# Kernel optimization log

Hardware: AMD Instinct MI355X
Metric: run time of the kernel (lower is better)

## Reference

```python
import jax, jax.numpy as jnp
import numpy as np

H = 512      # hidden_size
R = 47       # response_size
TR = 2       # treat_size
B = 128
T = 512


def _uniform(key, shape, k):
    return jax.random.uniform(key, shape, jnp.float32, -k, k)


def setup_inputs() -> dict:
    key = jax.random.key(0)
    ks = jax.random.split(key, 20)
    kinit = 1.0 / np.sqrt(H)
    inp = {
        "x_r": jax.random.normal(ks[0], (B, T, R), jnp.float32),
        "x_t": jax.random.normal(ks[1], (B, T, TR), jnp.float32),
        # r_rnn: 2-layer LSTM, input size R+TR=49 (torch gate order i,f,g,o)
        "r_Wih0": _uniform(ks[2], (4 * H, R + TR), kinit),
        "r_Whh0": _uniform(ks[3], (4 * H, H), kinit),
        "r_b0": _uniform(ks[4], (4 * H,), kinit),  # b_ih + b_hh fused
        "r_Wih1": _uniform(ks[5], (4 * H, H), kinit),
        "r_Whh1": _uniform(ks[6], (4 * H, H), kinit),
        "r_b1": _uniform(ks[7], (4 * H,), kinit),
        # t_rnn: 2-layer LSTM, input size 2*R+TR=96
        "t_Wih0": _uniform(ks[8], (4 * H, 2 * R + TR), kinit),
        "t_Whh0": _uniform(ks[9], (4 * H, H), kinit),
        "t_b0": _uniform(ks[10], (4 * H,), kinit),
        "t_Wih1": _uniform(ks[11], (4 * H, H), kinit),
        "t_Whh1": _uniform(ks[12], (4 * H, H), kinit),
        "t_b1": _uniform(ks[13], (4 * H,), kinit),
        # output linears
        "Wr": _uniform(ks[14], (R, H), kinit),
        "br": _uniform(ks[15], (R,), kinit),
        "Wt": _uniform(ks[16], (TR, H), kinit),
        "bt": _uniform(ks[17], (TR,), kinit),
    }
    return inp


def _lstm_cell(x, h, c, Wih, Whh, b):
    gates = x @ Wih.T + h @ Whh.T + b          # [B, 4H]
    i, f, g, o = jnp.split(gates, 4, axis=-1)
    c = jax.nn.sigmoid(f) * c + jax.nn.sigmoid(i) * jnp.tanh(g)
    h = jax.nn.sigmoid(o) * jnp.tanh(c)
    return h, c


def reference(x_r, x_t, r_Wih0, r_Whh0, r_b0, r_Wih1, r_Whh1, r_b1,
              t_Wih0, t_Whh0, t_b0, t_Wih1, t_Whh1, t_b1, Wr, br, Wt, bt):
    b = x_r.shape[0]
    z = jnp.zeros((b, H), x_r.dtype)
    carry0 = (z, z, z, z, z, z, z, z)  # (h,c) for 2 layers of r_rnn and t_rnn

    def step(carry, rt):
        hr0, cr0, hr1, cr1, ht0, ct0, ht1, ct1 = carry
        r, t = rt
        r_input = jnp.concatenate([r, t], axis=-1)          # [B, 49]
        hr0, cr0 = _lstm_cell(r_input, hr0, cr0, r_Wih0, r_Whh0, r_b0)
        hr1, cr1 = _lstm_cell(hr0, hr1, cr1, r_Wih1, r_Whh1, r_b1)
        r_out = hr1 @ Wr.T + br                             # [B, 47]
        t_input = jnp.concatenate([r_input, r_out], axis=-1)  # [B, 96]
        ht0, ct0 = _lstm_cell(t_input, ht0, ct0, t_Wih0, t_Whh0, t_b0)
        ht1, ct1 = _lstm_cell(ht0, ht1, ct1, t_Wih1, t_Whh1, t_b1)
        t_out = ht1 @ Wt.T + bt                             # [B, 2]
        return (hr0, cr0, hr1, cr1, ht0, ct0, ht1, ct1), (r_out, t_out)

    xs = (jnp.swapaxes(x_r, 0, 1), jnp.swapaxes(x_t, 0, 1))  # time-major [T,B,.]
    _, (r_seq, t_seq) = jax.lax.scan(step, carry0, xs)
    # back to batch-first, like the module's final permute(1,0,2)
    return jnp.swapaxes(r_seq, 0, 1), jnp.swapaxes(t_seq, 0, 1)
```

## Files before the change

kernel.cpp:

```cpp
#include <hip/hip_runtime.h>


typedef _Float16 half_t;
typedef _Float16 half8 __attribute__((ext_vector_type(8)));
typedef float floatx4 __attribute__((ext_vector_type(4)));
typedef unsigned long long ull_t;

#define OFF_W0 0
#define OFF_W1 131072
#define OFF_W2 1179648
#define OFF_W3 2228224
#define OFF_W4 3276800
#define OFF_W5 3407872
#define OFF_W6 3538944
#define OFF_W7 4587520
#define OFF_W8 5636096
#define OFF_W9 6684672
#define OFF_W10 6709248
#define W_TOTAL 6717440
#define H_BASE  6717440
#define RO_BASE 7241728
#define HALF_TOTAL 7258112
#define STATE_BYTE_OFF (H_BASE * 2)
#define C_BYTE_OFF (HALF_TOTAL * 2)
#define BAR_BYTE_OFF 15564800
#define X16_BYTE_OFF (BAR_BYTE_OFF + 4096)
#define WS_NEED_X16 ((unsigned long long)X16_BYTE_OFF + 8388608ull)
#define STATE_BYTES (X16_BYTE_OFF - STATE_BYTE_OFF)

#define NBLK 256
#define TOUT_BASE (128 * 512 * 47)

__device__ __forceinline__ floatx4 mfma16(half8 a, half8 b, floatx4 c) {
  return __builtin_amdgcn_mfma_f32_16x16x32_f16(a, b, c, 0, 0, 0);
}

__device__ __forceinline__ float fast_sig(float x) {
  x = fminf(fmaxf(x, -30.f), 30.f);
  float e = __expf(-x);
  return __builtin_amdgcn_rcpf(1.f + e);
}
__device__ __forceinline__ float fast_tanh(float x) {
  x = fminf(fmaxf(x, -15.f), 15.f);
  float e = __expf(-2.f * x);
  return (1.f - e) * __builtin_amdgcn_rcpf(1.f + e);
}

template <int N>
__device__ __forceinline__ void coh_stage(half8 (&bb)[N], const half_t* p) {
#pragma unroll
  for (int ks = 0; ks < N; ++ks)
    asm volatile("global_load_dwordx4 %0, %1, off sc0 sc1"
                 : "=v"(bb[ks])
                 : "v"(p + ks * 32));
}
__device__ __forceinline__ void drain_vm() {
  asm volatile("s_waitcnt vmcnt(0)" ::: "memory");
  __builtin_amdgcn_sched_barrier(0);
}

__device__ __forceinline__ void store_h4_coh(half_t* p, half_t h0, half_t h1,
                                             half_t h2, half_t h3) {
  union { ull_t u; _Float16 h[4]; } x;
  x.h[0] = h0; x.h[1] = h1; x.h[2] = h2; x.h[3] = h3;
  __hip_atomic_store((ull_t*)p, x.u, __ATOMIC_RELAXED,
                     __HIP_MEMORY_SCOPE_AGENT);
}

__device__ __forceinline__ void poll_llc(const unsigned* p, unsigned target,
                                         int pace) {
  for (;;) {
    unsigned v;
    asm volatile("global_load_dword %0, %1, off sc0 sc1\ns_waitcnt vmcnt(0)"
                 : "=v"(v) : "v"(p));
    if (v >= target) return;
    if (pace == 1) __builtin_amdgcn_s_sleep(1);
    else __builtin_amdgcn_s_sleep(3);
  }
}

template <int NT, int NSEG, int LDW>
__device__ __forceinline__ void gemm_staged(const half_t* __restrict__ W,
                                            const int* wrow,
                                            const half8 (&bb)[NSEG], int lk,
                                            int l15, floatx4 (&acc)[NT]) {
#pragma unroll
  for (int ks = 0; ks < NSEG; ++ks) {
    const int kb = ks * 32 + lk;
#pragma unroll
    for (int n = 0; n < NT; ++n) {
      half8 a = *(const half8*)(W + (long)(wrow[n] + l15) * LDW + kb);
      acc[n] = mfma16(a, bb[ks], acc[n]);
    }
  }
}

__device__ __forceinline__ void gemm_plain2(const half_t* __restrict__ W,
                                            const int* wrow,
                                            const half_t* __restrict__ xb,
                                            int lk, int l15, floatx4 (&acc)[4]) {
#pragma unroll
  for (int ks = 0; ks < 2; ++ks) {
    const int kb = ks * 32 + lk;
    half8 b = *(const half8*)(xb + kb);
#pragma unroll
    for (int n = 0; n < 4; ++n) {
      half8 a = *(const half8*)(W + (long)(wrow[n] + l15) * 64 + kb);
      acc[n] = mfma16(a, b, acc[n]);
    }
  }
}

__device__ __forceinline__ void gemm_xf(const float* __restrict__ xr,
                                        const float* __restrict__ xt, int t,
                                        int batch, const half_t* __restrict__ W,
                                        const int* wrow, int lk, int l15,
                                        floatx4 (&acc)[4]) {
#pragma unroll
  for (int ks = 0; ks < 2; ++ks) {
    const int kb = ks * 32 + lk;
    half8 b;
    const long base = (long)batch * 512 + t;
#pragma unroll
    for (int j = 0; j < 8; ++j) {
      const int kk = kb + j;
      float f = 0.f;
      if (kk < 47) f = xr[base * 47 + kk];
      else if (kk < 49) f = xt[base * 2 + (kk - 47)];
      b[j] = (half_t)f;
    }
#pragma unroll
    for (int n = 0; n < 4; ++n) {
      half8 a = *(const half8*)(W + (long)(wrow[n] + l15) * 64 + kb);
      acc[n] = mfma16(a, b, acc[n]);
    }
  }
}

__device__ __forceinline__ void lstm_epi_sw(floatx4 (&acc)[4],
                                            const float* __restrict__ bias,
                                            float* __restrict__ cst,
                                            half_t* __restrict__ hdst,
                                            int batch, int hcol0) {
  const floatx4 bI = *(const floatx4*)(bias + hcol0);
  const floatx4 bF = *(const floatx4*)(bias + 512 + hcol0);
  const floatx4 bG = *(const floatx4*)(bias + 1024 + hcol0);
  const floatx4 bO = *(const floatx4*)(bias + 1536 + hcol0);
  const int off = batch * 512 + hcol0;
  floatx4 cold = *(floatx4*)(cst + off);
  floatx4 cn;
  half_t hn[4];
#pragma unroll
  for (int r = 0; r < 4; ++r) {
    const float gi = acc[0][r] + bI[r];
    const float gf = acc[1][r] + bF[r];
    const float gg = acc[2][r] + bG[r];
    const float go = acc[3][r] + bO[r];
    cn[r] = fast_sig(gf) * cold[r] + fast_sig(gi) * fast_tanh(gg);
    hn[r] = (half_t)(fast_sig(go) * fast_tanh(cn[r]));
  }
  *(floatx4*)(cst + off) = cn;
  store_h4_coh(hdst + off, hn[0], hn[1], hn[2], hn[3]);
}

__global__ __launch_bounds__(256, 1) void adrnn_persist(
    const float* __restrict__ xr, const float* __restrict__ xt,
    const float* __restrict__ b_r0, const float* __restrict__ b_r1,
    const float* __restrict__ b_t0, const float* __restrict__ b_t1,
    const float* __restrict__ brv, const float* __restrict__ btv,
    half_t* __restrict__ w16, float* __restrict__ cbase,
    float* __restrict__ out, unsigned* bar, const half_t* __restrict__ x16,
    int use_x16) {
  const int bid = blockIdx.x;
  const int tid = threadIdx.x;
  const int lane = tid & 63;
  const int w = tid >> 6;
  const int l15 = lane & 15;
  const int q = lane >> 4;
  const int lk = q * 8;
  half_t* H = w16 + H_BASE;
  half_t* RO = w16 + RO_BASE;
#define HB(cell, p) (H + (((cell)*2 + (p)) << 16))

  const int stage = (bid & 7) >> 1;
  const int csHi = bid & 1;
  const int bh = (bid >> 3) & 1;
  const int csLo = bid >> 4;
  const int cs = csHi * 16 + csLo;
  const int sub = cs * 2 + bh;
  const int c0 = cs * 16;
  const int batch = bh * 64 + w * 16 + l15;
  const int hboff = batch * 512;
  const int hcol0 = c0 + q * 4;
  const int sd = (stage == 0) ? 0 : (stage == 1) ? 1 : (stage == 2) ? 3 : 4;
  int wrow[4] = {c0, 512 + c0, 1024 + c0, 1536 + c0};
  const int flat = sub * 4 + w;

  unsigned* larr = bar + (bid & 7) * 32;
  unsigned* garr = bar + 256;
  unsigned* lgen = bar + 288 + (bid & 7) * 32;

  for (int k = 0; k < 517; ++k) {
    const int par = k & 1, pq = par ^ 1;
    const int t = k - sd;
    if (t >= 0 && t < 512) {
      floatx4 acc[4] = {};
      if (stage == 0) {
        half8 b0[16];
        coh_stage<16>(b0, HB(0, pq) + hboff + lk);
        drain_vm();
        if (use_x16)
          gemm_plain2(w16 + OFF_W0, wrow, x16 + t * 8192 + batch * 64, lk, l15, acc);
        else
          gemm_xf(xr, xt, t, batch, w16 + OFF_W0, wrow, lk, l15, acc);
        gemm_staged<4, 16, 512>(w16 + OFF_W1, wrow, b0, lk, l15, acc);
        lstm_epi_sw(acc, b_r0, cbase + 0 * 65536, HB(0, par), batch, hcol0);
      } else if (stage == 1) {
        half8 b0[16], b1[16];
        coh_stage<16>(b0, HB(0, pq) + hboff + lk);
        coh_stage<16>(b1, HB(1, pq) + hboff + lk);
        drain_vm();
        gemm_staged<4, 16, 512>(w16 + OFF_W2, wrow, b0, lk, l15, acc);
        gemm_staged<4, 16, 512>(w16 + OFF_W3, wrow, b1, lk, l15, acc);
        lstm_epi_sw(acc, b_r1, cbase + 1 * 65536, HB(1, par), batch, hcol0);
      } else if (stage == 2) {
        half8 bro[2], b2[16];
        coh_stage<2>(bro, RO + pq * 8192 + batch * 64 + lk);
        coh_stage<16>(b2, HB(2, pq) + hboff + lk);
        drain_vm();
        if (use_x16)
          gemm_plain2(w16 + OFF_W4, wrow, x16 + t * 8192 + batch * 64, lk, l15, acc);
        else
          gemm_xf(xr, xt, t, batch, w16 + OFF_W4, wrow, lk, l15, acc);
        gemm_staged<4, 2, 64>(w16 + OFF_W5, wrow, bro, lk, l15, acc);
        gemm_staged<4, 16, 512>(w16 + OFF_W6, wrow, b2, lk, l15, acc);
        lstm_epi_sw(acc, b_t0, cbase + 2 * 65536, HB(2, par), batch, hcol0);
      } else {
        half8 b0[16], b1[16];
        coh_stage<16>(b0, HB(2, pq) + hboff + lk);
        coh_stage<16>(b1, HB(3, pq) + hboff + lk);
        drain_vm();
        gemm_staged<4, 16, 512>(w16 + OFF_W7, wrow, b0, lk, l15, acc);
        gemm_staged<4, 16, 512>(w16 + OFF_W8, wrow, b1, lk, l15, acc);
        lstm_epi_sw(acc, b_t1, cbase + 3 * 65536, HB(3, par), batch, hcol0);
      }
    }
    if (stage == 0 && flat < 32) {
      if (flat < 24) {
        const int tr = k - 2;
        if (tr >= 0 && tr < 512) {
          const int n = flat >> 3, btl = flat & 7;
          const int rb = btl * 16 + l15;
          half8 bs[16];
          coh_stage<16>(bs, HB(1, pq) + rb * 512 + lk);
          drain_vm();
          int wr1[1] = {n * 16};
          floatx4 accr[1] = {};
          gemm_staged<1, 16, 512>(w16 + OFF_W9, wr1, bs, lk, l15, accr);
          const int wc0 = n * 16 + q * 4;
          half_t ro4[4];
#pragma unroll
          for (int r = 0; r < 4; ++r) {
            const int wc = wc0 + r;
            float v = 0.f;
            if (wc < 47) {
              v = accr[0][r] + brv[wc];
              out[((long)rb * 512 + tr) * 47 + wc] = v;
            }
            ro4[r] = (half_t)v;
          }
          store_h4_coh(RO + par * 8192 + rb * 64 + wc0, ro4[0], ro4[1], ro4[2], ro4[3]);
        }
      } else {
        const int tt = k - 5;
        if (tt >= 0 && tt < 512) {
          const int btl = flat - 24;
          const int rb = btl * 16 + l15;
          half8 bs[16];
          coh_stage<16>(bs, HB(3, pq) + rb * 512 + lk);
          drain_vm();
          int wt1[1] = {0};
          floatx4 accw[1] = {};
          gemm_staged<1, 16, 512>(w16 + OFF_W10, wt1, bs, lk, l15, accw);
          if (q == 0) {
#pragma unroll
            for (int r = 0; r < 2; ++r)
              out[TOUT_BASE + ((long)rb * 512 + tt) * 2 + r] = accw[0][r] + btv[r];
          }
        }
      }
    }
    asm volatile("s_waitcnt vmcnt(0)" ::: "memory");
    __syncthreads();
    if (tid == 0) {
      const unsigned ku = (unsigned)k + 1u;
      (void)__hip_atomic_fetch_add(larr, 1u, __ATOMIC_RELAXED,
                                   __HIP_MEMORY_SCOPE_AGENT);
      if (bid < 8) {
        poll_llc(larr, 32u * ku, 1);
        (void)__hip_atomic_fetch_add(garr, 1u, __ATOMIC_RELAXED,
                                     __HIP_MEMORY_SCOPE_AGENT);
        poll_llc(garr, 8u * ku, 1);
        (void)__hip_atomic_fetch_add(lgen, 1u, __ATOMIC_RELAXED,
                                     __HIP_MEMORY_SCOPE_AGENT);
      } else {
        poll_llc(lgen, ku, 3);
      }
    }
    __syncthreads();
    asm volatile("" ::: "memory");
  }
#undef HB
}

__global__ __launch_bounds__(256) void conv_w(
    const float* __restrict__ rWih0, const float* __restrict__ rWhh0,
    const float* __restrict__ rWih1, const float* __restrict__ rWhh1,
    const float* __restrict__ tWih0, const float* __restrict__ tWhh0,
    const float* __restrict__ tWih1, const float* __restrict__ tWhh1,
    const float* __restrict__ Wr, const float* __restrict__ Wt,
    half_t* __restrict__ w16) {
  const int idx = blockIdx.x * 256 + threadIdx.x;
  if (idx >= W_TOTAL) return;
  float v = 0.f;
  if (idx < OFF_W1) {
    int n = idx >> 6, kk = idx & 63;
    if (kk < 49) v = rWih0[n * 49 + kk];
  } else if (idx < OFF_W2) {
    int r = idx - OFF_W1; v = rWhh0[r];
  } else if (idx < OFF_W3) {
    int r = idx - OFF_W2; v = rWih1[r];
  } else if (idx < OFF_W4) {
    int r = idx - OFF_W3; v = rWhh1[r];
  } else if (idx < OFF_W5) {
    int r = idx - OFF_W4; int n = r >> 6, kk = r & 63;
    if (kk < 49) v = tWih0[n * 96 + kk];
  } else if (idx < OFF_W6) {
    int r = idx - OFF_W5; int n = r >> 6, kk = r & 63;
    if (kk < 47) v = tWih0[n * 96 + 49 + kk];
  } else if (idx < OFF_W7) {
    int r = idx - OFF_W6; v = tWhh0[r];
  } else if (idx < OFF_W8) {
    int r = idx - OFF_W7; v = tWih1[r];
  } else if (idx < OFF_W9) {
    int r = idx - OFF_W8; v = tWhh1[r];
  } else if (idx < OFF_W10) {
    int r = idx - OFF_W9; int n = r >> 9, kk = r & 511;
    if (n < 47) v = Wr[n * 512 + kk];
  } else {
    int r = idx - OFF_W10; int n = r >> 9, kk = r & 511;
    if (n < 2) v = Wt[n * 512 + kk];
  }
  w16[idx] = (half_t)v;
}

__global__ __launch_bounds__(256) void conv_x(const float* __restrict__ xr,
                                              const float* __restrict__ xt,
                                              half_t* __restrict__ x16) {
  const int idx = blockIdx.x * 256 + threadIdx.x;
  if (idx >= 512 * 128 * 64) return;
  const int kk = idx & 63;
  const int row = (idx >> 6) & 127;
  const int t = idx >> 13;
  float v = 0.f;
  if (kk < 47) v = xr[(row * 512 + t) * 47 + kk];
  else if (kk < 49) v = xt[(row * 512 + t) * 2 + (kk - 47)];
  x16[idx] = (half_t)v;
}

extern "C" void kernel_launch(void* const* d_in, const int* in_sizes, int n_in,
                              void* d_out, int out_size, void* d_ws,
                              size_t ws_size, hipStream_t stream) {
  const float* xr = (const float*)d_in[0];
  const float* xt = (const float*)d_in[1];
  const float* rWih0 = (const float*)d_in[2];
  const float* rWhh0 = (const float*)d_in[3];
  const float* r_b0 = (const float*)d_in[4];
  const float* rWih1 = (const float*)d_in[5];
  const float* rWhh1 = (const float*)d_in[6];
  const float* r_b1 = (const float*)d_in[7];
  const float* tWih0 = (const float*)d_in[8];
  const float* tWhh0 = (const float*)d_in[9];
  const float* t_b0 = (const float*)d_in[10];
  const float* tWih1 = (const float*)d_in[11];
  const float* tWhh1 = (const float*)d_in[12];
  const float* t_b1 = (const float*)d_in[13];
  const float* Wr = (const float*)d_in[14];
  const float* br = (const float*)d_in[15];
  const float* Wt = (const float*)d_in[16];
  const float* bt = (const float*)d_in[17];

  half_t* w16 = (half_t*)d_ws;
  float* cbase = (float*)((char*)d_ws + C_BYTE_OFF);
  unsigned* bar = (unsigned*)((char*)d_ws + BAR_BYTE_OFF);
  half_t* x16 = (half_t*)((char*)d_ws + X16_BYTE_OFF);
  float* out = (float*)d_out;
  int use_x16 = (ws_size >= WS_NEED_X16) ? 1 : 0;

  (void)hipMemsetAsync((char*)d_ws + STATE_BYTE_OFF, 0, STATE_BYTES, stream);

  conv_w<<<(W_TOTAL + 255) / 256, 256, 0, stream>>>(
      rWih0, rWhh0, rWih1, rWhh1, tWih0, tWhh0, tWih1, tWhh1, Wr, Wt, w16);
  if (use_x16)
    conv_x<<<(512 * 128 * 64) / 256, 256, 0, stream>>>(xr, xt, x16);

  adrnn_persist<<<NBLK, 256, 0, stream>>>(xr, xt, r_b0, r_b1, t_b0, t_b1, br,
                                          bt, w16, cbase, out, bar, x16,
                                          use_x16);
}
```

Before: 10.82 ms.

## Stage hidden-state slabs in LDS and remap blocks to share batch tiles

Each block now owns a 16-batch tile and 64 hidden columns (one 16-column slice per wave) instead of 64 batches by 16 columns. Each step it loads the shared 16x512 hidden-state slab once from coherent global memory into XOR-swizzled LDS, and all waves read their B operands from there. Before, every wave pulled its own 16-batch row slice through sc0 sc1 loads into 16 registers per operand. The goal is less redundant coherent global traffic and lower VGPR pressure. The cost is an extra __syncthreads and an LDS round trip per step, and each wave now reads a different slice of the weight matrix.

After: 9.214 ms. 1.17x faster.

```diff
diff --git a/kernel.cpp b/kernel.cpp
--- a/kernel.cpp
+++ b/kernel.cpp
@@ -34,7 +34,6 @@
 __device__ __forceinline__ floatx4 mfma16(half8 a, half8 b, floatx4 c) {
   return __builtin_amdgcn_mfma_f32_16x16x32_f16(a, b, c, 0, 0, 0);
 }
-
 __device__ __forceinline__ float fast_sig(float x) {
   x = fminf(fmaxf(x, -30.f), 30.f);
   float e = __expf(-x);
@@ -51,14 +50,12 @@
 #pragma unroll
   for (int ks = 0; ks < N; ++ks)
     asm volatile("global_load_dwordx4 %0, %1, off sc0 sc1"
-                 : "=v"(bb[ks])
-                 : "v"(p + ks * 32));
+                 : "=v"(bb[ks]) : "v"(p + ks * 32));
 }
 __device__ __forceinline__ void drain_vm() {
   asm volatile("s_waitcnt vmcnt(0)" ::: "memory");
   __builtin_amdgcn_sched_barrier(0);
 }
-
 __device__ __forceinline__ void store_h4_coh(half_t* p, half_t h0, half_t h1,
                                              half_t h2, half_t h3) {
   union { ull_t u; _Float16 h[4]; } x;
@@ -66,24 +63,61 @@
   __hip_atomic_store((ull_t*)p, x.u, __ATOMIC_RELAXED,
                      __HIP_MEMORY_SCOPE_AGENT);
 }
-
-__device__ __forceinline__ void poll_llc(const unsigned* p, unsigned target,
-                                         int pace) {
+template <int PACE>
+__device__ __forceinline__ void poll_llc(const unsigned* p, unsigned target) {
   for (;;) {
     unsigned v;
     asm volatile("global_load_dword %0, %1, off sc0 sc1\ns_waitcnt vmcnt(0)"
                  : "=v"(v) : "v"(p));
     if (v >= target) return;
-    if (pace == 1) __builtin_amdgcn_s_sleep(1);
-    else __builtin_amdgcn_s_sleep(3);
+    __builtin_amdgcn_s_sleep(PACE);
+  }
+}
+
+__device__ __forceinline__ void slab_issue(half8 (&tmp)[4],
+                                           const half_t* __restrict__ src,
+                                           int tid) {
+#pragma unroll
+  for (int j = 0; j < 4; ++j) {
+    const int u = tid + j * 256;
+    asm volatile("global_load_dwordx4 %0, %1, off sc0 sc1"
+                 : "=v"(tmp[j]) : "v"(src + (u >> 6) * 512 + (u & 63) * 8));
+  }
+}
+__device__ __forceinline__ void slab_write(char* base, const half8 (&tmp)[4],
+                                           int tid) {
+#pragma unroll
+  for (int j = 0; j < 4; ++j) {
+    const int u = tid + j * 256;
+    const int row = u >> 6, seg = u & 63;
+    *(half8*)(base + row * 1024 + ((seg * 16) ^ ((row & 7) << 4))) = tmp[j];
   }
 }
 
 template <int NT, int NSEG, int LDW>
-__device__ __forceinline__ void gemm_staged(const half_t* __restrict__ W,
-                                            const int* wrow,
-                                            const half8 (&bb)[NSEG], int lk,
-                                            int l15, floatx4 (&acc)[NT]) {
+__device__ __forceinline__ void gemm_lb(const half_t* __restrict__ W,
+                                        const int* wrow, const char* ldsb,
+                                        int lk, int q, int l15,
+                                        floatx4 (&acc)[NT]) {
+  const int bbase = l15 * 1024;
+  const int bxor = (l15 & 7) << 4;
+#pragma unroll
+  for (int ks = 0; ks < NSEG; ++ks) {
+    const int kb = ks * 32 + lk;
+    half8 b = *(const half8*)(ldsb + bbase + ((q * 16 + ks * 64) ^ bxor));
+#pragma unroll
+    for (int n = 0; n < NT; ++n) {
+      half8 a = *(const half8*)(W + (long)(wrow[n] + l15) * LDW + kb);
+      acc[n] = mfma16(a, b, acc[n]);
+    }
+  }
+}
+
+template <int NT, int NSEG, int LDW>
+__device__ __forceinline__ void gemm_regB(const half_t* __restrict__ W,
+                                          const int* wrow,
+                                          const half8 (&bb)[NSEG], int lk,
+                                          int l15, floatx4 (&acc)[NT]) {
 #pragma unroll
   for (int ks = 0; ks < NSEG; ++ks) {
     const int kb = ks * 32 + lk;
@@ -95,10 +129,10 @@
   }
 }
 
-__device__ __forceinline__ void gemm_plain2(const half_t* __restrict__ W,
-                                            const int* wrow,
-                                            const half_t* __restrict__ xb,
-                                            int lk, int l15, floatx4 (&acc)[4]) {
+__device__ __forceinline__ void gemm_x16(const half_t* __restrict__ W,
+                                         const int* wrow,
+                                         const half_t* __restrict__ xb, int lk,
+                                         int l15, floatx4 (&acc)[4]) {
 #pragma unroll
   for (int ks = 0; ks < 2; ++ks) {
     const int kb = ks * 32 + lk;
@@ -110,7 +144,6 @@
     }
   }
 }
-
 __device__ __forceinline__ void gemm_xf(const float* __restrict__ xr,
                                         const float* __restrict__ xt, int t,
                                         int batch, const half_t* __restrict__ W,
@@ -171,6 +204,10 @@
     half_t* __restrict__ w16, float* __restrict__ cbase,
     float* __restrict__ out, unsigned* bar, const half_t* __restrict__ x16,
     int use_x16) {
+  __shared__ half8 lds_v[2048];
+  char* lds0 = (char*)lds_v;
+  char* lds1 = lds0 + 16384;
+
   const int bid = blockIdx.x;
   const int tid = threadIdx.x;
   const int lane = tid & 63;
@@ -183,18 +220,19 @@
 #define HB(cell, p) (H + (((cell)*2 + (p)) << 16))
 
   const int stage = (bid & 7) >> 1;
-  const int csHi = bid & 1;
-  const int bh = (bid >> 3) & 1;
-  const int csLo = bid >> 4;
-  const int cs = csHi * 16 + csLo;
-  const int sub = cs * 2 + bh;
-  const int c0 = cs * 16;
-  const int batch = bh * 64 + w * 16 + l15;
-  const int hboff = batch * 512;
-  const int hcol0 = c0 + q * 4;
+  const int hgHi = bid & 1;
+  const int rr = bid >> 3;
+  const int hgLo = rr >> 3;
+  const int bg = rr & 7;
+  const int hg = hgHi * 4 + hgLo;
+  const int c0w = hg * 64 + w * 16;
+  const int b0 = bg * 16;
+  const int batch = b0 + l15;
+  const int hcol0 = c0w + q * 4;
   const int sd = (stage == 0) ? 0 : (stage == 1) ? 1 : (stage == 2) ? 3 : 4;
-  int wrow[4] = {c0, 512 + c0, 1024 + c0, 1536 + c0};
-  const int flat = sub * 4 + w;
+  int wrow[4] = {c0w, 512 + c0w, 1024 + c0w, 1536 + c0w};
+  const int flat = (hg * 8 + bg) * 4 + w;
+  const bool is_spare = (stage == 0 && hg < 2 && flat < 32);
 
   unsigned* larr = bar + (bid & 7) * 32;
   unsigned* garr = bar + 256;
@@ -203,49 +241,66 @@
   for (int k = 0; k < 517; ++k) {
     const int par = k & 1, pq = par ^ 1;
     const int t = k - sd;
-    if (t >= 0 && t < 512) {
+    const bool valid = (t >= 0 && t < 512);
+
+    if (valid) {
+      half8 s0[4], s1[4];
+      if (stage == 0) {
+        slab_issue(s0, HB(0, pq) + b0 * 512, tid);
+        drain_vm();
+        slab_write(lds0, s0, tid);
+      } else if (stage == 1) {
+        slab_issue(s0, HB(0, pq) + b0 * 512, tid);
+        slab_issue(s1, HB(1, pq) + b0 * 512, tid);
+        drain_vm();
+        slab_write(lds0, s0, tid);
+        slab_write(lds1, s1, tid);
+      } else if (stage == 2) {
+        slab_issue(s0, HB(2, pq) + b0 * 512, tid);
+        drain_vm();
+        slab_write(lds0, s0, tid);
+      } else {
+        slab_issue(s0, HB(2, pq) + b0 * 512, tid);
+        slab_issue(s1, HB(3, pq) + b0 * 512, tid);
+        drain_vm();
+        slab_write(lds0, s0, tid);
+        slab_write(lds1, s1, tid);
+      }
+    }
+    __syncthreads();
+
+    if (valid) {
       floatx4 acc[4] = {};
       if (stage == 0) {
-        half8 b0[16];
-        coh_stage<16>(b0, HB(0, pq) + hboff + lk);
+        if (use_x16)
+          gemm_x16(w16 + OFF_W0, wrow, x16 + (long)t * 8192 + batch * 64, lk, l15, acc);
+        else
+          gemm_xf(xr, xt, t, batch, w16 + OFF_W0, wrow, lk, l15, acc);
+        gemm_lb<4, 16, 512>(w16 + OFF_W1, wrow, lds0, lk, q, l15, acc);
+        lstm_epi_sw(acc, b_r0, cbase + 0 * 65536, HB(0, par), batch, hcol0);
+      } else if (stage == 1) {
+        gemm_lb<4, 16, 512>(w16 + OFF_W2, wrow, lds0, lk, q, l15, acc);
+        gemm_lb<4, 16, 512>(w16 + OFF_W3, wrow, lds1, lk, q, l15, acc);
+        lstm_epi_sw(acc, b_r1, cbase + 1 * 65536, HB(1, par), batch, hcol0);
+      } else if (stage == 2) {
+        half8 bro[2];
+        coh_stage<2>(bro, RO + pq * 8192 + batch * 64 + lk);
         drain_vm();
         if (use_x16)
-          gemm_plain2(w16 + OFF_W0, wrow, x16 + t * 8192 + batch * 64, lk, l15, acc);
-        else
-          gemm_xf(xr, xt, t, batch, w16 + OFF_W0, wrow, lk, l15, acc);
-        gemm_staged<4, 16, 512>(w16 + OFF_W1, wrow, b0, lk, l15, acc);
-        lstm_epi_sw(acc, b_r0, cbase + 0 * 65536, HB(0, par), batch, hcol0);
-      } else if (stage == 1) {
-        half8 b0[16], b1[16];
-        coh_stage<16>(b0, HB(0, pq) + hboff + lk);
-        coh_stage<16>(b1, HB(1, pq) + hboff + lk);
-        drain_vm();
-        gemm_staged<4, 16, 512>(w16 + OFF_W2, wrow, b0, lk, l15, acc);
-        gemm_staged<4, 16, 512>(w16 + OFF_W3, wrow, b1, lk, l15, acc);
-        lstm_epi_sw(acc, b_r1, cbase + 1 * 65536, HB(1, par), batch, hcol0);
-      } else if (stage == 2) {
-        half8 bro[2], b2[16];
-        coh_stage<2>(bro, RO + pq * 8192 + batch * 64 + lk);
-        coh_stage<16>(b2, HB(2, pq) + hboff + lk);
-        drain_vm();
-        if (use_x16)
-          gemm_plain2(w16 + OFF_W4, wrow, x16 + t * 8192 + batch * 64, lk, l15, acc);
+          gemm_x16(w16 + OFF_W4, wrow, x16 + (long)t * 8192 + batch * 64, lk, l15, acc);
         else
           gemm_xf(xr, xt, t, batch, w16 + OFF_W4, wrow, lk, l15, acc);
-        gemm_staged<4, 2, 64>(w16 + OFF_W5, wrow, bro, lk, l15, acc);
-        gemm_staged<4, 16, 512>(w16 + OFF_W6, wrow, b2, lk, l15, acc);
+        gemm_regB<4, 2, 64>(w16 + OFF_W5, wrow, bro, lk, l15, acc);
+        gemm_lb<4, 16, 512>(w16 + OFF_W6, wrow, lds0, lk, q, l15, acc);
         lstm_epi_sw(acc, b_t0, cbase + 2 * 65536, HB(2, par), batch, hcol0);
       } else {
-        half8 b0[16], b1[16];
-        coh_stage<16>(b0, HB(2, pq) + hboff + lk);
-        coh_stage<16>(b1, HB(3, pq) + hboff + lk);
-        drain_vm();
-        gemm_staged<4, 16, 512>(w16 + OFF_W7, wrow, b0, lk, l15, acc);
-        gemm_staged<4, 16, 512>(w16 + OFF_W8, wrow, b1, lk, l15, acc);
+        gemm_lb<4, 16, 512>(w16 + OFF_W7, wrow, lds0, lk, q, l15, acc);
+        gemm_lb<4, 16, 512>(w16 + OFF_W8, wrow, lds1, lk, q, l15, acc);
         lstm_epi_sw(acc, b_t1, cbase + 3 * 65536, HB(3, par), batch, hcol0);
       }
     }
-    if (stage == 0 && flat < 32) {
+
+    if (is_spare) {
       if (flat < 24) {
         const int tr = k - 2;
         if (tr >= 0 && tr < 512) {
@@ -256,7 +311,7 @@
           drain_vm();
           int wr1[1] = {n * 16};
           floatx4 accr[1] = {};
-          gemm_staged<1, 16, 512>(w16 + OFF_W9, wr1, bs, lk, l15, accr);
+          gemm_regB<1, 16, 512>(w16 + OFF_W9, wr1, bs, lk, l15, accr);
           const int wc0 = n * 16 + q * 4;
           half_t ro4[4];
 #pragma unroll
@@ -281,7 +336,7 @@
           drain_vm();
           int wt1[1] = {0};
           floatx4 accw[1] = {};
-          gemm_staged<1, 16, 512>(w16 + OFF_W10, wt1, bs, lk, l15, accw);
+          gemm_regB<1, 16, 512>(w16 + OFF_W10, wt1, bs, lk, l15, accw);
           if (q == 0) {
 #pragma unroll
             for (int r = 0; r < 2; ++r)
@@ -290,6 +345,7 @@
         }
       }
     }
+
     asm volatile("s_waitcnt vmcnt(0)" ::: "memory");
     __syncthreads();
     if (tid == 0) {
@@ -297,14 +353,14 @@
       (void)__hip_atomic_fetch_add(larr, 1u, __ATOMIC_RELAXED,
                                    __HIP_MEMORY_SCOPE_AGENT);
       if (bid < 8) {
-        poll_llc(larr, 32u * ku, 1);
+        poll_llc<1>(larr, 32u * ku);
         (void)__hip_atomic_fetch_add(garr, 1u, __ATOMIC_RELAXED,
                                      __HIP_MEMORY_SCOPE_AGENT);
-        poll_llc(garr, 8u * ku, 1);
+        poll_llc<1>(garr, 8u * ku);
         (void)__hip_atomic_fetch_add(lgen, 1u, __ATOMIC_RELAXED,
                                      __HIP_MEMORY_SCOPE_AGENT);
       } else {
-        poll_llc(lgen, ku, 3);
+        poll_llc<3>(lgen, ku);
       }
     }
     __syncthreads();
```
